# Kernel optimization log

Measured on AMD Instinct MI355X. Metric: run time of the kernel, lower is better.

## Reference

```python
import jax, jax.numpy as jnp
import numpy as np

B, S, L, D = 16, 32, 256, 768   # batch, sentences, seq_len, bert hidden
P, T = 16, 4                    # predicates per sentence, tokens per predicate span
VOCAB = 30522
PAD = 1                         # hardcoded pad id in original (`!= 1`)


def setup_inputs() -> dict:
    key = jax.random.key(0)
    ks = jax.random.split(key, 7)
    sentence_ids = jax.random.randint(ks[0], (B, S, L), 0, VOCAB, dtype=jnp.int32)
    sentence_attention_masks = jax.random.randint(ks[1], (B, S, L), 0, 2, dtype=jnp.int32)

    def sample_span_ids(k):
        # sample predicate/arg token ids from the actual sentence tokens so matches occur,
        k1, k2 = jax.random.split(k)
        pos = jax.random.randint(k1, (B, S, P, T), 0, L)
        ids = jnp.take_along_axis(sentence_ids[:, :, None, :], pos.reshape(B, S, P * T)[:, :, None, :], axis=-1)
        ids = ids.reshape(B, S, P, T)
        pad_mask = jax.random.uniform(k2, (B, S, P, T)) < 0.25
        return jnp.where(pad_mask, PAD, ids).astype(jnp.int32)

    predicate_ids = sample_span_ids(ks[2])
    arg0_ids = sample_span_ids(ks[3])
    arg1_ids = sample_span_ids(ks[4])
    # frozen BERT last_hidden_state (encoder is no_grad & vendor-optimized; stubbed as input)
    token_embeddings = jax.random.normal(ks[5], (B, S, L, D), dtype=jnp.float32)
    return {
        "sentence_ids": sentence_ids,
        "sentence_attention_masks": sentence_attention_masks,
        "predicate_ids": predicate_ids,
        "arg0_ids": arg0_ids,
        "arg1_ids": arg1_ids,
        "token_embeddings": token_embeddings,
    }


def _arg_embedding(ids, sentence_ids, attn, emb):
    # ids: [B,S,P,T]; emb: [B,S,L,D]
    # matches[b,s,p,t,l] = (sent[l]==ids[t]) & ids[t]!=PAD & attn[l]
    valid = ids != PAD                                              # [B,S,P,T]
    m = (sentence_ids[:, :, None, None, :] == ids[..., None])       # [B,S,P,T,L]
    m = m & valid[..., None] & (attn[:, :, None, None, :] != 0)
    # a sentence token matching multiple span tokens is counted multiple times
    # (original flattens (t,l) match indices and means over all of them)
    cnt = m.sum(axis=3).astype(emb.dtype)                           # [B,S,P,L]
    num = jnp.einsum('bspl,bsld->bspd', cnt, emb)                   # [B,S,P,D]
    den = cnt.sum(axis=-1, keepdims=True)                           # [B,S,P,1]
    return jnp.where(den > 0, num / jnp.maximum(den, 1.0), 0.0)


def reference(sentence_ids, sentence_attention_masks, predicate_ids, arg0_ids, arg1_ids, token_embeddings):
    mask = sentence_attention_masks.astype(token_embeddings.dtype)  # [B,S,L]
    sent_sum = jnp.einsum('bsl,bsld->bsd', mask, token_embeddings)
    tok_cnt = jnp.clip(mask.sum(axis=-1, keepdims=True), 1.0, None)
    sentence_embeddings_avg = sent_sum / tok_cnt                    # [B,S,D]

    predicate_embeddings = _arg_embedding(predicate_ids, sentence_ids, sentence_attention_masks, token_embeddings)
    arg0_embeddings = _arg_embedding(arg0_ids, sentence_ids, sentence_attention_masks, token_embeddings)
    arg1_embeddings = _arg_embedding(arg1_ids, sentence_ids, sentence_attention_masks, token_embeddings)
    return (sentence_embeddings_avg, predicate_embeddings, arg0_embeddings, arg1_embeddings)
```

## Files before the change

### kernel.cpp

```cpp
#include <hip/hip_runtime.h>

constexpr int BS_TOTAL = 16 * 32;
constexpr int L = 256;
constexpr int D = 768;
constexpr int P = 16;
constexpr int T = 4;
constexpr int PAD = 1;
constexpr int NROWS = 3 * P;

constexpr int GROUPS = 4;
constexpr int LANES  = D / 4;
constexpr int NTHREADS = GROUPS * LANES;

__global__ __launch_bounds__(NTHREADS, 1) void srl_kernel(
    const int*   __restrict__ sent_ids,
    const int*   __restrict__ attn_mask,
    const int*   __restrict__ pred_ids,
    const int*   __restrict__ arg0_ids,
    const int*   __restrict__ arg1_ids,
    const float* __restrict__ emb,
    float*       __restrict__ out)
{
    const int bs = blockIdx.x;
    const int t  = threadIdx.x;
    const int g  = t / LANES;
    const int c  = t % LANES;

    __shared__ int            s_span[NROWS * T];
    __shared__ int            s_act[L];
    __shared__ unsigned short s_list[NROWS][L];
    __shared__ int            s_rown[NROWS];
    __shared__ int            s_nact;
    __shared__ float          s_part[(GROUPS - 1) * D];

    if (t < NROWS) s_rown[t] = 0;
    if (t == NTHREADS - 1) s_nact = 0;

    if (t < 64)       s_span[t] = pred_ids[bs * 64 + t];
    else if (t < 128) s_span[t] = arg0_ids[bs * 64 + (t - 64)];
    else if (t < 192) s_span[t] = arg1_ids[bs * 64 + (t - 128)];

    int key = -1;
    if (t < L) {
        const int sid = sent_ids[bs * L + t];
        const int am  = attn_mask[bs * L + t];
        key = (am != 0) ? sid : -1;
    }
    __syncthreads();

    if (t < L) {
        if (key >= 0) {
            const int pos = atomicAdd(&s_nact, 1);
            s_act[pos] = t;
        }
        for (int r = 0; r < NROWS; ++r) {
            int cnt = 0;
            #pragma unroll
            for (int k = 0; k < T; ++k) {
                const int id = s_span[r * T + k];
                cnt += (id != PAD && id == key) ? 1 : 0;
            }
            if (cnt > 0) {
                const int pos = atomicAdd(&s_rown[r], 1);
                s_list[r][pos] = (unsigned short)((cnt << 8) | t);
            }
        }
    }
    __syncthreads();

    const size_t ebase = (size_t)bs * (L * D);
    const int nact = s_nact;

    float4 acc = make_float4(0.f, 0.f, 0.f, 0.f);
    #pragma unroll 4
    for (int i = g; i < nact; i += GROUPS) {
        const int l = s_act[i];
        const float4 v = *(const float4*)(emb + ebase + (size_t)l * D + 4 * c);
        acc.x += v.x; acc.y += v.y; acc.z += v.z; acc.w += v.w;
    }
    if (g > 0) *(float4*)&s_part[(g - 1) * D + 4 * c] = acc;
    __syncthreads();
    if (g == 0) {
        #pragma unroll
        for (int q = 0; q < GROUPS - 1; ++q) {
            const float4 o = *(const float4*)&s_part[q * D + 4 * c];
            acc.x += o.x; acc.y += o.y; acc.z += o.z; acc.w += o.w;
        }
        const float inv = 1.0f / (float)(nact > 0 ? nact : 1);
        float4 rr = make_float4(acc.x * inv, acc.y * inv, acc.z * inv, acc.w * inv);
        *(float4*)(out + (size_t)bs * D + 4 * c) = rr;
    }

    float* argbase = out + (size_t)BS_TOTAL * D;
    const size_t argstride = (size_t)BS_TOTAL * P * D;
    for (int r = g; r < NROWS; r += GROUPS) {
        const int n   = s_rown[r];
        const int typ = r >> 4;
        const int p   = r & (P - 1);
        float* op = argbase + (size_t)typ * argstride + ((size_t)bs * P + p) * D + 4 * c;
        float4 a = make_float4(0.f, 0.f, 0.f, 0.f);
        int den = 0;
        for (int i = 0; i < n; ++i) {
            const unsigned int e = s_list[r][i];
            const int   l = (int)(e & 255u);
            const int   w = (int)(e >> 8);
            den += w;
            const float wf = (float)w;
            const float4 v = *(const float4*)(emb + ebase + (size_t)l * D + 4 * c);
            a.x += wf * v.x; a.y += wf * v.y; a.z += wf * v.z; a.w += wf * v.w;
        }
        if (n > 0) {
            const float inv = 1.0f / (float)den;
            a.x *= inv; a.y *= inv; a.z *= inv; a.w *= inv;
        }
        *(float4*)op = a;
    }
}

extern "C" void kernel_launch(void* const* d_in, const int* in_sizes, int n_in,
                              void* d_out, int out_size, void* d_ws, size_t ws_size,
                              hipStream_t stream) {
    srl_kernel<<<dim3(BS_TOTAL), dim3(NTHREADS), 0, stream>>>(
        (const int*)d_in[0],
        (const int*)d_in[1],
        (const int*)d_in[2],
        (const int*)d_in[3],
        (const int*)d_in[4],
        (const float*)d_in[5],
        (float*)d_out);
}
```

Baseline: 534.7 us.

## Split fused kernel into metadata, split-sentence-sum, reduce and per-row span kernels

Replaces the single kernel (one block per sentence) with four launches. A metadata pass writes the active-token and match lists to workspace. A sentence-sum pass splits across 8 blocks per sentence and is followed by a reduction kernel. The span pass uses one block per (sentence, row). This creates far more blocks to fill the GPU and hide memory latency, at the cost of extra launches, workspace traffic, and embeddings that are re-read across blocks instead of within one.

```diff
diff --git a/kernel.cpp b/kernel.cpp
--- a/kernel.cpp
+++ b/kernel.cpp
@@ -1,4 +1,7 @@
 #include <hip/hip_runtime.h>
+
+typedef unsigned short ushort_t;
+typedef unsigned int uint_t;
 
 constexpr int BS_TOTAL = 16 * 32;
 constexpr int L = 256;
@@ -7,125 +10,179 @@
 constexpr int T = 4;
 constexpr int PAD = 1;
 constexpr int NROWS = 3 * P;
+constexpr int SPLIT = 8;
+constexpr int C4 = D / 4;
 
-constexpr int GROUPS = 4;
-constexpr int LANES  = D / 4;
-constexpr int NTHREADS = GROUPS * LANES;
+constexpr size_t WS_PART = 0;
+constexpr size_t WS_NACT = WS_PART + (size_t)BS_TOTAL * SPLIT * D * 4;
+constexpr size_t WS_ACT  = WS_NACT + (size_t)BS_TOTAL * 4;
+constexpr size_t WS_N    = WS_ACT  + (size_t)BS_TOTAL * L * 2;
+constexpr size_t WS_DEN  = WS_N    + (size_t)BS_TOTAL * NROWS * 4;
+constexpr size_t WS_ENT  = WS_DEN  + (size_t)BS_TOTAL * NROWS * 4;
 
-__global__ __launch_bounds__(NTHREADS, 1) void srl_kernel(
-    const int*   __restrict__ sent_ids,
-    const int*   __restrict__ attn_mask,
-    const int*   __restrict__ pred_ids,
-    const int*   __restrict__ arg0_ids,
-    const int*   __restrict__ arg1_ids,
-    const float* __restrict__ emb,
-    float*       __restrict__ out)
+__global__ __launch_bounds__(256, 1) void k_meta(
+    const int* __restrict__ sent_ids, const int* __restrict__ attn_mask,
+    const int* __restrict__ pred_ids, const int* __restrict__ arg0_ids,
+    const int* __restrict__ arg1_ids,
+    int* __restrict__ ws_nact, ushort_t* __restrict__ ws_act,
+    int* __restrict__ ws_n, int* __restrict__ ws_den, ushort_t* __restrict__ ws_ent)
 {
     const int bs = blockIdx.x;
     const int t  = threadIdx.x;
-    const int g  = t / LANES;
-    const int c  = t % LANES;
 
-    __shared__ int            s_span[NROWS * T];
-    __shared__ int            s_act[L];
-    __shared__ unsigned short s_list[NROWS][L];
-    __shared__ int            s_rown[NROWS];
-    __shared__ int            s_nact;
-    __shared__ float          s_part[(GROUPS - 1) * D];
+    __shared__ int      s_span[NROWS * T];
+    __shared__ ushort_t s_act[L];
+    __shared__ ushort_t s_list[NROWS][L];
+    __shared__ int      s_rown[NROWS];
+    __shared__ int      s_den[NROWS];
+    __shared__ int      s_nact;
 
-    if (t < NROWS) s_rown[t] = 0;
-    if (t == NTHREADS - 1) s_nact = 0;
+    if (t < NROWS) { s_rown[t] = 0; s_den[t] = 0; }
+    if (t == 255) s_nact = 0;
 
     if (t < 64)       s_span[t] = pred_ids[bs * 64 + t];
     else if (t < 128) s_span[t] = arg0_ids[bs * 64 + (t - 64)];
     else if (t < 192) s_span[t] = arg1_ids[bs * 64 + (t - 128)];
 
-    int key = -1;
-    if (t < L) {
-        const int sid = sent_ids[bs * L + t];
-        const int am  = attn_mask[bs * L + t];
-        key = (am != 0) ? sid : -1;
-    }
+    const int sid = sent_ids[bs * L + t];
+    const int am  = attn_mask[bs * L + t];
+    const int key = (am != 0) ? sid : -1;
     __syncthreads();
 
-    if (t < L) {
-        if (key >= 0) {
-            const int pos = atomicAdd(&s_nact, 1);
-            s_act[pos] = t;
+    if (key >= 0) {
+        const int pos = atomicAdd(&s_nact, 1);
+        s_act[pos] = (ushort_t)t;
+    }
+    for (int r = 0; r < NROWS; ++r) {
+        int cnt = 0;
+        #pragma unroll
+        for (int k = 0; k < T; ++k) {
+            const int id = s_span[r * T + k];
+            cnt += (id != PAD && id == key) ? 1 : 0;
         }
-        for (int r = 0; r < NROWS; ++r) {
-            int cnt = 0;
-            #pragma unroll
-            for (int k = 0; k < T; ++k) {
-                const int id = s_span[r * T + k];
-                cnt += (id != PAD && id == key) ? 1 : 0;
-            }
-            if (cnt > 0) {
-                const int pos = atomicAdd(&s_rown[r], 1);
-                s_list[r][pos] = (unsigned short)((cnt << 8) | t);
-            }
+        if (cnt > 0) {
+            const int pos = atomicAdd(&s_rown[r], 1);
+            s_list[r][pos] = (ushort_t)((cnt << 8) | t);
+            atomicAdd(&s_den[r], cnt);
         }
     }
     __syncthreads();
 
+    if (t == 0) ws_nact[bs] = s_nact;
+    ws_act[bs * L + t] = s_act[t];
+    if (t < NROWS) {
+        ws_n[bs * NROWS + t]   = s_rown[t];
+        ws_den[bs * NROWS + t] = s_den[t];
+    }
+    for (int r = 0; r < NROWS; ++r) {
+        if (t < s_rown[r]) ws_ent[((size_t)bs * NROWS + r) * L + t] = s_list[r][t];
+    }
+}
+
+__global__ __launch_bounds__(192, 1) void k_sent_partial(
+    const float* __restrict__ emb, const int* __restrict__ ws_nact,
+    const ushort_t* __restrict__ ws_act, float* __restrict__ ws_part)
+{
+    const int bs = blockIdx.x;
+    const int sp = blockIdx.y;
+    const int t  = threadIdx.x;
+
+    __shared__ ushort_t s_act[L];
+    __shared__ int s_n;
+    if (t == 0) s_n = ws_nact[bs];
+    if (t < L / 2) ((uint_t*)s_act)[t] = ((const uint_t*)(ws_act + bs * L))[t];
+    __syncthreads();
+
+    const int nact = s_n;
     const size_t ebase = (size_t)bs * (L * D);
-    const int nact = s_nact;
-
     float4 acc = make_float4(0.f, 0.f, 0.f, 0.f);
     #pragma unroll 4
-    for (int i = g; i < nact; i += GROUPS) {
+    for (int i = sp; i < nact; i += SPLIT) {
         const int l = s_act[i];
-        const float4 v = *(const float4*)(emb + ebase + (size_t)l * D + 4 * c);
+        const float4 v = *(const float4*)(emb + ebase + (size_t)l * D + 4 * t);
         acc.x += v.x; acc.y += v.y; acc.z += v.z; acc.w += v.w;
     }
-    if (g > 0) *(float4*)&s_part[(g - 1) * D + 4 * c] = acc;
+    *(float4*)(ws_part + ((size_t)bs * SPLIT + sp) * D + 4 * t) = acc;
+}
+
+__global__ __launch_bounds__(192, 1) void k_sent_reduce(
+    const float* __restrict__ ws_part, const int* __restrict__ ws_nact,
+    float* __restrict__ out)
+{
+    const int bs = blockIdx.x;
+    const int t  = threadIdx.x;
+    float4 s = make_float4(0.f, 0.f, 0.f, 0.f);
+    #pragma unroll
+    for (int sp = 0; sp < SPLIT; ++sp) {
+        const float4 v = *(const float4*)(ws_part + ((size_t)bs * SPLIT + sp) * D + 4 * t);
+        s.x += v.x; s.y += v.y; s.z += v.z; s.w += v.w;
+    }
+    const int nact = ws_nact[bs];
+    const float inv = 1.0f / (float)(nact > 0 ? nact : 1);
+    float4 r = make_float4(s.x * inv, s.y * inv, s.z * inv, s.w * inv);
+    *(float4*)(out + (size_t)bs * D + 4 * t) = r;
+}
+
+__global__ __launch_bounds__(192, 1) void k_spans(
+    const float* __restrict__ emb, const int* __restrict__ ws_n,
+    const int* __restrict__ ws_den, const ushort_t* __restrict__ ws_ent,
+    float* __restrict__ out)
+{
+    const int bs = blockIdx.x;
+    const int r  = blockIdx.y;
+    const int t  = threadIdx.x;
+
+    __shared__ ushort_t s_e[L];
+    __shared__ int s_n, s_d;
+    if (t == 0) { s_n = ws_n[bs * NROWS + r]; s_d = ws_den[bs * NROWS + r]; }
+    if (t < L / 2) ((uint_t*)s_e)[t] = ((const uint_t*)(ws_ent + ((size_t)bs * NROWS + r) * L))[t];
     __syncthreads();
-    if (g == 0) {
-        #pragma unroll
-        for (int q = 0; q < GROUPS - 1; ++q) {
-            const float4 o = *(const float4*)&s_part[q * D + 4 * c];
-            acc.x += o.x; acc.y += o.y; acc.z += o.z; acc.w += o.w;
-        }
-        const float inv = 1.0f / (float)(nact > 0 ? nact : 1);
-        float4 rr = make_float4(acc.x * inv, acc.y * inv, acc.z * inv, acc.w * inv);
-        *(float4*)(out + (size_t)bs * D + 4 * c) = rr;
+
+    const int n = s_n;
+    const size_t ebase = (size_t)bs * (L * D);
+    float4 a = make_float4(0.f, 0.f, 0.f, 0.f);
+    for (int i = 0; i < n; ++i) {
+        const uint_t e = s_e[i];
+        const int l = (int)(e & 255u);
+        const float w = (float)(e >> 8);
+        const float4 v = *(const float4*)(emb + ebase + (size_t)l * D + 4 * t);
+        a.x += w * v.x; a.y += w * v.y; a.z += w * v.z; a.w += w * v.w;
     }
+    const float inv = (n > 0) ? 1.0f / (float)s_d : 0.0f;
+    a.x *= inv; a.y *= inv; a.z *= inv; a.w *= inv;
 
-    float* argbase = out + (size_t)BS_TOTAL * D;
-    const size_t argstride = (size_t)BS_TOTAL * P * D;
-    for (int r = g; r < NROWS; r += GROUPS) {
-        const int n   = s_rown[r];
-        const int typ = r >> 4;
-        const int p   = r & (P - 1);
-        float* op = argbase + (size_t)typ * argstride + ((size_t)bs * P + p) * D + 4 * c;
-        float4 a = make_float4(0.f, 0.f, 0.f, 0.f);
-        int den = 0;
-        for (int i = 0; i < n; ++i) {
-            const unsigned int e = s_list[r][i];
-            const int   l = (int)(e & 255u);
-            const int   w = (int)(e >> 8);
-            den += w;
-            const float wf = (float)w;
-            const float4 v = *(const float4*)(emb + ebase + (size_t)l * D + 4 * c);
-            a.x += wf * v.x; a.y += wf * v.y; a.z += wf * v.z; a.w += wf * v.w;
-        }
-        if (n > 0) {
-            const float inv = 1.0f / (float)den;
-            a.x *= inv; a.y *= inv; a.z *= inv; a.w *= inv;
-        }
-        *(float4*)op = a;
-    }
+    const int typ = r >> 4;
+    const int p   = r & (P - 1);
+    float* op = out + (size_t)BS_TOTAL * D + (size_t)typ * BS_TOTAL * P * D
+              + ((size_t)bs * P + p) * D + 4 * t;
+    *(float4*)op = a;
 }
 
 extern "C" void kernel_launch(void* const* d_in, const int* in_sizes, int n_in,
                               void* d_out, int out_size, void* d_ws, size_t ws_size,
                               hipStream_t stream) {
-    srl_kernel<<<dim3(BS_TOTAL), dim3(NTHREADS), 0, stream>>>(
-        (const int*)d_in[0],
-        (const int*)d_in[1],
-        (const int*)d_in[2],
-        (const int*)d_in[3],
-        (const int*)d_in[4],
-        (const float*)d_in[5],
-        (float*)d_out);
+    const int*   sent = (const int*)d_in[0];
+    const int*   attn = (const int*)d_in[1];
+    const int*   pred = (const int*)d_in[2];
+    const int*   a0   = (const int*)d_in[3];
+    const int*   a1   = (const int*)d_in[4];
+    const float* emb  = (const float*)d_in[5];
+    float*       out  = (float*)d_out;
+
+    char* ws = (char*)d_ws;
+    float*    ws_part = (float*)(ws + WS_PART);
+    int*      ws_nact = (int*)(ws + WS_NACT);
+    ushort_t* ws_act  = (ushort_t*)(ws + WS_ACT);
+    int*      ws_n    = (int*)(ws + WS_N);
+    int*      ws_den  = (int*)(ws + WS_DEN);
+    ushort_t* ws_ent  = (ushort_t*)(ws + WS_ENT);
+
+    k_meta<<<dim3(BS_TOTAL), dim3(256), 0, stream>>>(
+        sent, attn, pred, a0, a1, ws_nact, ws_act, ws_n, ws_den, ws_ent);
+    k_sent_partial<<<dim3(BS_TOTAL, SPLIT), dim3(C4), 0, stream>>>(
+        emb, ws_nact, ws_act, ws_part);
+    k_sent_reduce<<<dim3(BS_TOTAL), dim3(C4), 0, stream>>>(
+        ws_part, ws_nact, out);
+    k_spans<<<dim3(BS_TOTAL, NROWS), dim3(C4), 0, stream>>>(
+        emb, ws_n, ws_den, ws_ent, out);
 }
```

New measurement: 557.8 us. 4.3% more time.
